# Performance work log

Hardware: AMD Instinct MI355X
Metric: run time of the kernel (lower is better)

## Reference

```python
import jax, jax.numpy as jnp
import numpy as np

B, T, V, H = 32, 256, 16, 256


def _layer_norm(x, g, b, eps=1e-5):
    m = jnp.mean(x, axis=-1, keepdims=True)
    v = jnp.mean(jnp.square(x - m), axis=-1, keepdims=True)
    return (x - m) * jax.lax.rsqrt(v + eps) * g + b


def setup_inputs() -> dict:
    keys = iter(jax.random.split(jax.random.key(0), 16))

    def nrm(shape, s=0.02):
        return (jax.random.normal(next(keys), shape, dtype=jnp.float32) * s).astype(jnp.float32)

    return {
        "x": nrm((B, T, V, H), 1.0),
        "context": nrm((B, T, H), 1.0),
        "joint_Wa": nrm((V * H, H)),
        "joint_ba": jnp.zeros((H,), jnp.float32),
        "joint_Wc": nrm((H, H)),
        "joint_Wi": nrm((H, H)),
        "joint_bi": jnp.zeros((H,), jnp.float32),
        "joint_Wglu": nrm((H, 2 * V)),
        "joint_bglu": jnp.zeros((2 * V,), jnp.float32),
        "joint_Wskip": nrm((V * H, V)),
        "joint_bskip": jnp.zeros((V,), jnp.float32),
        "joint_ln_g": jnp.ones((V,), jnp.float32),
        "joint_ln_b": jnp.zeros((V,), jnp.float32),
        "var_Wa": nrm((V, H, H)),
        "var_ba": jnp.zeros((V, H), jnp.float32),
        "var_Wi": nrm((V, H, H)),
        "var_bi": jnp.zeros((V, H), jnp.float32),
        "var_Wglu": nrm((V, H, 2 * H)),
        "var_bglu": jnp.zeros((V, 2 * H), jnp.float32),
        "var_ln_g": jnp.ones((V, H), jnp.float32),
        "var_ln_b": jnp.zeros((V, H), jnp.float32),
    }


def reference(x, context, joint_Wa, joint_ba, joint_Wc, joint_Wi, joint_bi,
              joint_Wglu, joint_bglu, joint_Wskip, joint_bskip,
              joint_ln_g, joint_ln_b,
              var_Wa, var_ba, var_Wi, var_bi, var_Wglu, var_bglu,
              var_ln_g, var_ln_b):
    b, t, v, h = x.shape
    Xi = x.reshape(b, t, v * h)  # flatten last two dims

    # ---- joint GRN (with context) producing variable logits [b,t,v] ----
    a = Xi @ joint_Wa + joint_ba + context @ joint_Wc
    a = jax.nn.elu(a)
    i = a @ joint_Wi + joint_bi
    g = i @ joint_Wglu + joint_bglu
    g1, g2 = jnp.split(g, 2, axis=-1)  # GLU: first half gated by sigmoid(second)
    glu_out = g1 * jax.nn.sigmoid(g2)
    skip = Xi @ joint_Wskip + joint_bskip  # out_size != in_size -> skip projection
    sparse_weights = jax.nn.softmax(_layer_norm(glu_out + skip, joint_ln_g, joint_ln_b), axis=-1)

    # ---- per-variable GRNs, batched over the variable axis ----
    av = jax.nn.elu(jnp.einsum('btvh,vhk->btvk', x, var_Wa) + var_ba)
    iv = jnp.einsum('btvh,vhk->btvk', av, var_Wi) + var_bi
    gv = jnp.einsum('btvh,vhd->btvd', iv, var_Wglu) + var_bglu
    gv1, gv2 = jnp.split(gv, 2, axis=-1)
    tv = _layer_norm(gv1 * jax.nn.sigmoid(gv2) + x, var_ln_g, var_ln_b)  # [b,t,v,h]

    # stack(dim=-1) + matmul with weights == weighted sum over variables
    variable_ctx = jnp.einsum('btvh,btv->bth', tv, sparse_weights)
    return variable_ctx, sparse_weights
```

## Files before the change

### kernel.cpp

```cpp
#include <hip/hip_runtime.h>

typedef unsigned short u16;
typedef __attribute__((ext_vector_type(8))) __bf16 bf16x8;
typedef __attribute__((ext_vector_type(4))) float f32x4;
typedef __attribute__((ext_vector_type(8))) u16 u16x8;

__device__ __forceinline__ u16 f2b(float f) {
  union { float f; unsigned u; } v; v.f = f;
  return (u16)((v.u + 0x7fffu + ((v.u >> 16) & 1u)) >> 16);
}
__device__ __forceinline__ float b2f(u16 h) {
  union { unsigned u; float f; } v; v.u = ((unsigned)h) << 16;
  return v.f;
}
__device__ __forceinline__ f32x4 mfma16(bf16x8 a, bf16x8 b, f32x4 c) {
  return __builtin_amdgcn_mfma_f32_16x16x32_bf16(a, b, c, 0, 0, 0);
}
__device__ __forceinline__ void gl_lds16(const void* g, void* l) {
  __builtin_amdgcn_global_load_lds(
      (const __attribute__((address_space(1))) void*)g,
      (__attribute__((address_space(3))) void*)l, 16, 0, 0);
}
__device__ __forceinline__ u16x8 cvt8(float4 a, float4 b) {
  u16x8 o;
  o[0] = f2b(a.x); o[1] = f2b(a.y); o[2] = f2b(a.z); o[3] = f2b(a.w);
  o[4] = f2b(b.x); o[5] = f2b(b.y); o[6] = f2b(b.z); o[7] = f2b(b.w);
  return o;
}
__device__ __forceinline__ u16x8 cvt8v(f32x4 a, f32x4 b) {
  u16x8 o;
  o[0] = f2b(a[0]); o[1] = f2b(a[1]); o[2] = f2b(a[2]); o[3] = f2b(a[3]);
  o[4] = f2b(b[0]); o[5] = f2b(b[1]); o[6] = f2b(b[2]); o[7] = f2b(b[3]);
  return o;
}

__global__ __launch_bounds__(256) void transpose_cast(
    const float* __restrict__ src, u16* __restrict__ dst,
    int R, int C, int dstStride, long srcBatch, long dstBatch)
{
  __shared__ float tile[32][33];
  src += (long)blockIdx.z * srcBatch;
  dst += (long)blockIdx.z * dstBatch;
  const int c0 = blockIdx.x * 32, r0 = blockIdx.y * 32;
  const int tx = threadIdx.x & 31, ty = threadIdx.x >> 5;
  for (int i = ty; i < 32; i += 8) {
    int r = r0 + i, cc = c0 + tx;
    if (r < R && cc < C) tile[i][tx] = src[(long)r * C + cc];
  }
  __syncthreads();
  for (int i = ty; i < 32; i += 8) {
    int cc = c0 + i, r = r0 + tx;
    if (cc < C && r < R) dst[(long)cc * dstStride + r] = f2b(tile[tx][i]);
  }
}

__global__ __launch_bounds__(256) void var_w_prep(
    const float* __restrict__ W, u16* __restrict__ dstbase, int rbase)
{
  const int v = blockIdx.x;
  const int kc = blockIdx.y;
  const int n = threadIdx.x;
  const float* src = W + (size_t)v * 65536 + (size_t)kc * 64 * 256 + n;
  u16* dst = dstbase + (size_t)v * 262144 + (size_t)(rbase + kc) * 16384;
#pragma unroll
  for (int l = 0; l < 8; ++l) {
    u16x8 o;
#pragma unroll
    for (int e = 0; e < 8; ++e) o[e] = f2b(src[(l * 8 + e) * 256]);
    const int chunk = n * 8 + (l ^ (n & 7));
    *(u16x8*)&dst[chunk * 8] = o;
  }
}

__global__ __launch_bounds__(256) void var_wglu_prep(
    const float* __restrict__ W, u16* __restrict__ dstbase)
{
  const int v = blockIdx.x;
  const int kc = blockIdx.y;
  u16* dst = dstbase + (size_t)v * 262144 + (size_t)(8 + kc) * 16384;
#pragma unroll
  for (int half = 0; half < 2; ++half) {
    const int n = threadIdx.x + half * 256;
    const float* src = W + (size_t)v * 131072 + (size_t)kc * 32 * 512 + n;
    const int s = n >> 1;
#pragma unroll
    for (int l = 0; l < 4; ++l) {
      u16x8 o;
#pragma unroll
      for (int e = 0; e < 8; ++e) o[e] = f2b(src[(l * 8 + e) * 512]);
      const int chunk = s * 8 + ((((n & 1) * 4 + l)) ^ (s & 7));
      *(u16x8*)&dst[chunk * 8] = o;
    }
  }
}

#define K1TOT 4352
__global__ __launch_bounds__(256, 3) void gemm1(
    const float* __restrict__ x, const float* __restrict__ ctx,
    const u16* __restrict__ bt1, const float* __restrict__ ba,
    const float* __restrict__ bskip, u16* __restrict__ a_bf, float* __restrict__ skip_f)
{
  __shared__ u16 As[32 * 64];
  __shared__ u16 Bs[288 * 64];
  const int tid = threadIdx.x;
  const int n0 = blockIdx.x * 32;
  const int w = tid >> 6, lane = tid & 63;
  const int q = lane >> 4, c = lane & 15;
  const int rt = w & 1, cg = w >> 1;
  const int t0 = cg ? 9 : 0;
  const int nt = cg ? 8 : 9;

  f32x4 acc[9];
#pragma unroll
  for (int i = 0; i < 9; ++i) acc[i] = f32x4{0.f, 0.f, 0.f, 0.f};

  const int sr = tid >> 3, sp = tid & 7;
  const int sl = sp ^ (sr & 7);

  for (int kb = 0; kb < K1TOT; kb += 64) {
    {
      const float* s = (kb < 4096)
          ? (x + (size_t)(n0 + sr) * 4096 + kb + sl * 8)
          : (ctx + (size_t)(n0 + sr) * 256 + (kb - 4096) + sl * 8);
      float4 v0 = ((const float4*)s)[0];
      float4 v1 = ((const float4*)s)[1];
      *(u16x8*)&As[tid * 8] = cvt8(v0, v1);
    }
#pragma unroll
    for (int i = 0; i < 9; ++i) {
      const int cb = (i * 4 + w) * 64;
      const int cid = cb + lane;
      const int row = cid >> 3, p = cid & 7;
      const int l = p ^ (row & 7);
      const u16* src = (row < 272) ? (bt1 + (size_t)row * K1TOT + kb + l * 8) : bt1;
      gl_lds16(src, &Bs[cb * 8]);
    }
    __syncthreads();
#pragma unroll
    for (int kk = 0; kk < 2; ++kk) {
      const int arow = rt * 16 + c;
      bf16x8 af = *(const bf16x8*)&As[(arow * 64 + kk * 32 + q * 8) ^ ((arow & 7) << 3)];
#pragma unroll
      for (int ti = 0; ti < 9; ++ti) {
        if (ti < nt) {
          const int n16 = (t0 + ti) * 16 + c;
          bf16x8 bfr = *(const bf16x8*)&Bs[(n16 * 64 + kk * 32 + q * 8) ^ ((n16 & 7) << 3)];
          acc[ti] = mfma16(af, bfr, acc[ti]);
        }
      }
    }
    __syncthreads();
  }
#pragma unroll
  for (int ti = 0; ti < 9; ++ti) {
    if (ti < nt) {
      const int col = (t0 + ti) * 16 + c;
#pragma unroll
      for (int j = 0; j < 4; ++j) {
        const long n = n0 + rt * 16 + q * 4 + j;
        float vv = acc[ti][j];
        if (col < 256) {
          vv += ba[col];
          vv = vv > 0.f ? vv : expm1f(vv);
          a_bf[n * 256 + col] = f2b(vv);
        } else {
          skip_f[n * 16 + (col - 256)] = vv + bskip[col - 256];
        }
      }
    }
  }
}

__global__ __launch_bounds__(256, 3) void gemm_i(
    const u16* __restrict__ a_bf, const u16* __restrict__ wiT,
    const float* __restrict__ bi, u16* __restrict__ i_bf)
{
  __shared__ u16 As[32 * 64];
  __shared__ u16 Bs[256 * 64];
  const int tid = threadIdx.x;
  const int n0 = blockIdx.x * 32;
  const int w = tid >> 6, lane = tid & 63;
  const int q = lane >> 4, c = lane & 15;
  const int rt = w & 1, cg = w >> 1;

  f32x4 acc[8];
#pragma unroll
  for (int i = 0; i < 8; ++i) acc[i] = f32x4{0.f, 0.f, 0.f, 0.f};

  for (int kb = 0; kb < 256; kb += 64) {
    {
      const int row = tid >> 3, p = tid & 7;
      const int l = p ^ (row & 7);
      gl_lds16(a_bf + (size_t)(n0 + row) * 256 + kb + l * 8, &As[w * 512]);
    }
#pragma unroll
    for (int i = 0; i < 8; ++i) {
      const int cb = (i * 4 + w) * 64;
      const int cid = cb + lane;
      const int row = cid >> 3, p = cid & 7;
      const int l = p ^ (row & 7);
      gl_lds16(wiT + (size_t)row * 256 + kb + l * 8, &Bs[cb * 8]);
    }
    __syncthreads();
#pragma unroll
    for (int kk = 0; kk < 2; ++kk) {
      const int arow = rt * 16 + c;
      bf16x8 af = *(const bf16x8*)&As[(arow * 64 + kk * 32 + q * 8) ^ ((arow & 7) << 3)];
#pragma unroll
      for (int ti = 0; ti < 8; ++ti) {
        const int n16 = (cg * 8 + ti) * 16 + c;
        bf16x8 bfr = *(const bf16x8*)&Bs[(n16 * 64 + kk * 32 + q * 8) ^ ((n16 & 7) << 3)];
        acc[ti] = mfma16(af, bfr, acc[ti]);
      }
    }
    __syncthreads();
  }
#pragma unroll
  for (int ti = 0; ti < 8; ++ti) {
    const int col = (cg * 8 + ti) * 16 + c;
    const float bb = bi[col];
#pragma unroll
    for (int j = 0; j < 4; ++j) {
      const long n = n0 + rt * 16 + q * 4 + j;
      i_bf[n * 256 + col] = f2b(acc[ti][j] + bb);
    }
  }
}

__global__ __launch_bounds__(256) void joint_tail(
    const u16* __restrict__ i_bf, const u16* __restrict__ wgluT,
    const float* __restrict__ bglu, const float* __restrict__ skip_f,
    const float* __restrict__ lng, const float* __restrict__ lnb,
    float* __restrict__ swout)
{
  __shared__ float wlds[32 * 257];
  __shared__ float ilds[4][256];
  const int tid = threadIdx.x;
  for (int jj = 0; jj < 32; ++jj) wlds[jj * 257 + tid] = b2f(wgluT[jj * 256 + tid]);
  const int w = tid >> 6, lane = tid & 63;
  const long n = (long)blockIdx.x * 4 + w;
  {
    const u16* src = i_bf + n * 256 + lane * 4;
    float4 f;
    f.x = b2f(src[0]); f.y = b2f(src[1]); f.z = b2f(src[2]); f.w = b2f(src[3]);
    *(float4*)&ilds[w][lane * 4] = f;
  }
  __syncthreads();
  const int cc32 = lane & 31;
  const int k0 = (lane >> 5) * 128;
  float acc = 0.f;
  for (int k = 0; k < 128; ++k) acc += ilds[w][k0 + k] * wlds[cc32 * 257 + k0 + k];
  acc += __shfl_xor(acc, 32, 64);
  const float gfull = acc + bglu[cc32];
  const int cc = lane & 15;
  const float g1 = __shfl(gfull, cc, 64);
  const float g2 = __shfl(gfull, cc + 16, 64);
  const float glu = g1 / (1.f + __expf(-g2));
  const float y = glu + skip_f[n * 16 + cc];
  float s = y, ss = y * y;
#pragma unroll
  for (int d = 1; d < 16; d <<= 1) { s += __shfl_xor(s, d, 64); ss += __shfl_xor(ss, d, 64); }
  const float m = s * (1.f / 16.f);
  const float var = ss * (1.f / 16.f) - m * m;
  const float t = (y - m) * rsqrtf(var + 1e-5f) * lng[cc] + lnb[cc];
  float mx = t;
#pragma unroll
  for (int d = 1; d < 16; d <<= 1) mx = fmaxf(mx, __shfl_xor(mx, d, 64));
  const float e = __expf(t - mx);
  float es = e;
#pragma unroll
  for (int d = 1; d < 16; d <<= 1) es += __shfl_xor(es, d, 64);
  if (lane < 16) swout[n * 16 + lane] = e / es;
}

__global__ __launch_bounds__(256) void reduce4(
    const float* __restrict__ part, float* __restrict__ out)
{
  const size_t i = ((size_t)blockIdx.x * 256 + threadIdx.x) * 4;
  float4 a = *(const float4*)(part + i);
  float4 b = *(const float4*)(part + i + 2097152);
  float4 c = *(const float4*)(part + i + 4194304);
  float4 d = *(const float4*)(part + i + 6291456);
  float4 o;
  o.x = a.x + b.x + c.x + d.x;
  o.y = a.y + b.y + c.y + d.y;
  o.z = a.z + b.z + c.z + d.z;
  o.w = a.w + b.w + c.w + d.w;
  *(float4*)(out + i) = o;
}

__global__ __launch_bounds__(1024, 1) void var_chain(
    const float* __restrict__ x, const u16* __restrict__ varw,
    const float* __restrict__ vba, const float* __restrict__ vbi,
    const float* __restrict__ vbglu, const float* __restrict__ vlng,
    const float* __restrict__ vlnb, const float* __restrict__ sw,
    float* __restrict__ outp)
{
  extern __shared__ u16 smem[];
  u16* const xt1 = smem;
  u16* const wtb = smem + 32768;
  float* const red   = (float*)(smem + 65536);
  float* const muinv = red + 1024;

  const int tid = threadIdx.x;
  const int w = tid >> 6, lane = tid & 63;
  const int q = lane >> 4, c = lane & 15;
  const int rt = w >> 2, cg = w & 3;
  const int vbase = blockIdx.x * 4;
  const int n0 = blockIdx.y * 128;

  f32x4 outacc[2][4];
#pragma unroll
  for (int p = 0; p < 2; ++p)
#pragma unroll
    for (int u = 0; u < 4; ++u) outacc[p][u] = f32x4{0.f, 0.f, 0.f, 0.f};

  auto STAGE = [&](int b, int tn) {
    const u16* tb = varw + (size_t)(vbase + (tn >> 4)) * 262144 + (size_t)(tn & 15) * 16384;
    u16* dst = wtb + (b << 14);
#pragma unroll
    for (int i = 0; i < 2; ++i) {
      const int cb = (i * 16 + w) * 64;
      gl_lds16(tb + (size_t)(cb + lane) * 8, dst + (size_t)cb * 8);
    }
  };
  auto XSTAGE = [&](int v) {
#pragma unroll
    for (int jj = 0; jj < 4; ++jj) {
      const int cid = jj * 1024 + tid;
      const int r = cid >> 5, p = cid & 31;
      const int l = (p & 24) | ((p & 7) ^ (r & 7));
      const f32x4* s = (const f32x4*)(x + (size_t)(n0 + r) * 4096 + (size_t)v * 256 + l * 8);
      f32x4 v0 = __builtin_nontemporal_load(s);
      f32x4 v1 = __builtin_nontemporal_load(s + 1);
      *(u16x8*)&xt1[cid * 8] = cvt8v(v0, v1);
    }
  };

  auto ROUND_TAIL = [&](int t) {
    __builtin_amdgcn_s_barrier();
    __builtin_amdgcn_sched_barrier(0);
    STAGE(t & 1, (t + 2 < 64) ? t + 2 : 63);
    __builtin_amdgcn_sched_barrier(0);
    asm volatile("s_waitcnt vmcnt(2)" ::: "memory");
    __builtin_amdgcn_sched_barrier(0);
    __builtin_amdgcn_s_barrier();
    __builtin_amdgcn_sched_barrier(0);
  };

  STAGE(0, 0);
  STAGE(1, 1);
  XSTAGE(vbase);
  __syncthreads();

  int t = 0;
  for (int vi = 0; vi < 4; ++vi) {
    const int v = vbase + vi;

    f32x4 acc2[2][4];
#pragma unroll
    for (int p = 0; p < 2; ++p)
#pragma unroll
      for (int ti = 0; ti < 4; ++ti) acc2[p][ti] = f32x4{0.f, 0.f, 0.f, 0.f};

    for (int kc = 0; kc < 4; ++kc, ++t) {
      const u16* wcur = wtb + ((t & 1) << 14);
      __builtin_amdgcn_s_setprio(1);
#pragma unroll
      for (int kk = 0; kk < 2; ++kk) {
        bf16x8 a[2];
#pragma unroll
        for (int p = 0; p < 2; ++p) {
          const int r = (rt * 2 + p) * 16 + c;
          a[p] = *(const bf16x8*)&xt1[(r * 256 + kc * 64 + kk * 32 + q * 8) ^ ((r & 7) << 3)];
        }
#pragma unroll
        for (int ti = 0; ti < 4; ++ti) {
          const int n16 = (cg * 4 + ti) * 16 + c;
          bf16x8 b = *(const bf16x8*)&wcur[(n16 * 64 + kk * 32 + q * 8) ^ ((n16 & 7) << 3)];
          acc2[0][ti] = mfma16(a[0], b, acc2[0][ti]);
          acc2[1][ti] = mfma16(a[1], b, acc2[1][ti]);
        }
      }
      __builtin_amdgcn_s_setprio(0);
      ROUND_TAIL(t);
    }
#pragma unroll
    for (int p = 0; p < 2; ++p)
#pragma unroll
      for (int ti = 0; ti < 4; ++ti) {
        const int col = (cg * 4 + ti) * 16 + c;
        const float bb = vba[v * 256 + col];
#pragma unroll
        for (int j = 0; j < 4; ++j) {
          const int row = (rt * 2 + p) * 16 + q * 4 + j;
          float vv = acc2[p][ti][j] + bb;
          vv = vv > 0.f ? vv : expm1f(vv);
          xt1[(row * 256 + col) ^ ((row & 7) << 3)] = f2b(vv);
        }
      }
    __syncthreads();

#pragma unroll
    for (int p = 0; p < 2; ++p)
#pragma unroll
      for (int ti = 0; ti < 4; ++ti) acc2[p][ti] = f32x4{0.f, 0.f, 0.f, 0.f};
    for (int kc = 0; kc < 4; ++kc, ++t) {
      const u16* wcur = wtb + ((t & 1) << 14);
      __builtin_amdgcn_s_setprio(1);
#pragma unroll
      for (int kk = 0; kk < 2; ++kk) {
        bf16x8 a[2];
#pragma unroll
        for (int p = 0; p < 2; ++p) {
          const int r = (rt * 2 + p) * 16 + c;
          a[p] = *(const bf16x8*)&xt1[(r * 256 + kc * 64 + kk * 32 + q * 8) ^ ((r & 7) << 3)];
        }
#pragma unroll
        for (int ti = 0; ti < 4; ++ti) {
          const int n16 = (cg * 4 + ti) * 16 + c;
          bf16x8 b = *(const bf16x8*)&wcur[(n16 * 64 + kk * 32 + q * 8) ^ ((n16 & 7) << 3)];
          acc2[0][ti] = mfma16(a[0], b, acc2[0][ti]);
          acc2[1][ti] = mfma16(a[1], b, acc2[1][ti]);
        }
      }
      __builtin_amdgcn_s_setprio(0);
      ROUND_TAIL(t);
    }
#pragma unroll
    for (int p = 0; p < 2; ++p)
#pragma unroll
      for (int ti = 0; ti < 4; ++ti) {
        const int col = (cg * 4 + ti) * 16 + c;
        const float bb = vbi[v * 256 + col];
#pragma unroll
        for (int j = 0; j < 4; ++j) {
          const int row = (rt * 2 + p) * 16 + q * 4 + j;
          xt1[(row * 256 + col) ^ ((row & 7) << 3)] = f2b(acc2[p][ti][j] + bb);
        }
      }
    __syncthreads();

    f32x4 acc3[2][8];
#pragma unroll
    for (int p = 0; p < 2; ++p)
#pragma unroll
      for (int u = 0; u < 8; ++u) acc3[p][u] = f32x4{0.f, 0.f, 0.f, 0.f};
    for (int kc = 0; kc < 8; ++kc, ++t) {
      const u16* wcur = wtb + ((t & 1) << 14);
      bf16x8 a[2];
#pragma unroll
      for (int p = 0; p < 2; ++p) {
        const int r = (rt * 2 + p) * 16 + c;
        a[p] = *(const bf16x8*)&xt1[(r * 256 + kc * 32 + q * 8) ^ ((r & 7) << 3)];
      }
      __builtin_amdgcn_s_setprio(1);
#pragma unroll
      for (int u = 0; u < 8; ++u) {
        const int ct = cg * 4 + (u & 3) + ((u >> 2) << 4);
        const int n = ct * 16 + c;
        const int idx = (n >> 1) * 64 + ((((n & 1) * 4 + q) ^ ((n >> 1) & 7)) * 8);
        bf16x8 b = *(const bf16x8*)&wcur[idx];
        acc3[0][u] = mfma16(a[0], b, acc3[0][u]);
        acc3[1][u] = mfma16(a[1], b, acc3[1][u]);
      }
      __builtin_amdgcn_s_setprio(0);
      ROUND_TAIL(t);
    }

    float b1v[4], b2v[4], lgv[4], lbv[4];
#pragma unroll
    for (int u = 0; u < 4; ++u) {
      const int col = cg * 64 + u * 16 + c;
      b1v[u] = vbglu[v * 512 + col];
      b2v[u] = vbglu[v * 512 + 256 + col];
      lgv[u] = vlng[v * 256 + col];
      lbv[u] = vlnb[v * 256 + col];
    }
    float rs[2][4], rss[2][4];
#pragma unroll
    for (int p = 0; p < 2; ++p)
#pragma unroll
      for (int j = 0; j < 4; ++j) { rs[p][j] = 0.f; rss[p][j] = 0.f; }
#pragma unroll
    for (int p = 0; p < 2; ++p)
#pragma unroll
      for (int u = 0; u < 4; ++u) {
        const int col = cg * 64 + u * 16 + c;
#pragma unroll
        for (int j = 0; j < 4; ++j) {
          const int row = (rt * 2 + p) * 16 + q * 4 + j;
          const float g1 = acc3[p][u][j] + b1v[u];
          const float g2 = acc3[p][u + 4][j] + b2v[u];
          const float glu = g1 / (1.f + __expf(-g2));
          const float resid = __builtin_nontemporal_load(
              &x[(size_t)(n0 + row) * 4096 + (size_t)v * 256 + col]);
          const float r = glu + resid;
          acc3[p][u][j] = r;
          rs[p][j] += r; rss[p][j] += r * r;
        }
      }
#pragma unroll
    for (int p = 0; p < 2; ++p)
#pragma unroll
      for (int j = 0; j < 4; ++j)
#pragma unroll
        for (int d = 1; d < 16; d <<= 1) {
          rs[p][j]  += __shfl_xor(rs[p][j], d, 64);
          rss[p][j] += __shfl_xor(rss[p][j], d, 64);
        }
    if (c == 0) {
#pragma unroll
      for (int p = 0; p < 2; ++p)
#pragma unroll
        for (int j = 0; j < 4; ++j) {
          const int row = (rt * 2 + p) * 16 + q * 4 + j;
          red[row * 8 + cg * 2]     = rs[p][j];
          red[row * 8 + cg * 2 + 1] = rss[p][j];
        }
    }
    __syncthreads();
    if (tid < 128) {
      float ms = 0.f, vs = 0.f;
#pragma unroll
      for (int ww = 0; ww < 4; ++ww) { ms += red[tid * 8 + ww * 2]; vs += red[tid * 8 + ww * 2 + 1]; }
      const float mm = ms * (1.f / 256.f);
      muinv[tid * 2]     = mm;
      muinv[tid * 2 + 1] = rsqrtf(vs * (1.f / 256.f) - mm * mm + 1e-5f);
    }
    __syncthreads();
#pragma unroll
    for (int p = 0; p < 2; ++p) {
#pragma unroll
      for (int j = 0; j < 4; ++j) {
        const int row = (rt * 2 + p) * 16 + q * 4 + j;
        const float mu = muinv[row * 2], inv = muinv[row * 2 + 1];
        const float wv = sw[(size_t)(n0 + row) * 16 + v];
#pragma unroll
        for (int u = 0; u < 4; ++u) {
          const float tv = (acc3[p][u][j] - mu) * inv * lgv[u] + lbv[u];
          outacc[p][u][j] += tv * wv;
        }
      }
    }
    __syncthreads();
    if (vi < 3) {
      XSTAGE(v + 1);
      __syncthreads();
    }
  }

  float* const dst = outp + (size_t)blockIdx.x * 2097152;
#pragma unroll
  for (int p = 0; p < 2; ++p)
#pragma unroll
    for (int u = 0; u < 4; ++u) {
      const int col = cg * 64 + u * 16 + c;
#pragma unroll
      for (int j = 0; j < 4; ++j) {
        const int row = (rt * 2 + p) * 16 + q * 4 + j;
        dst[(size_t)(n0 + row) * 256 + col] = outacc[p][u][j];
      }
    }
}

extern "C" void kernel_launch(void* const* d_in, const int* in_sizes, int n_in,
                              void* d_out, int out_size, void* d_ws, size_t ws_size,
                              hipStream_t stream) {
  const float* x     = (const float*)d_in[0];
  const float* ctx   = (const float*)d_in[1];
  const float* jWa   = (const float*)d_in[2];
  const float* jba   = (const float*)d_in[3];
  const float* jWc   = (const float*)d_in[4];
  const float* jWi   = (const float*)d_in[5];
  const float* jbi   = (const float*)d_in[6];
  const float* jWglu = (const float*)d_in[7];
  const float* jbglu = (const float*)d_in[8];
  const float* jWskip= (const float*)d_in[9];
  const float* jbskip= (const float*)d_in[10];
  const float* jlng  = (const float*)d_in[11];
  const float* jlnb  = (const float*)d_in[12];
  const float* vWa   = (const float*)d_in[13];
  const float* vba   = (const float*)d_in[14];
  const float* vWi   = (const float*)d_in[15];
  const float* vbi   = (const float*)d_in[16];
  const float* vWglu = (const float*)d_in[17];
  const float* vbglu = (const float*)d_in[18];
  const float* vlng  = (const float*)d_in[19];
  const float* vlnb  = (const float*)d_in[20];
  float* out = (float*)d_out;

  char* ws = (char*)d_ws;
  size_t off = 0;
  auto alloc = [&](size_t bytes) { void* p = ws + off; off += (bytes + 255) & ~(size_t)255; return p; };
  u16* bt1     = (u16*)alloc((size_t)272 * 4352 * 2);
  u16* wiT     = (u16*)alloc((size_t)256 * 256 * 2);
  u16* wgluT   = (u16*)alloc((size_t)32 * 256 * 2);
  u16* varw    = (u16*)alloc((size_t)16 * 262144 * 2);
  u16* a_bf    = (u16*)alloc((size_t)8192 * 256 * 2);
  u16* i_bf    = (u16*)alloc((size_t)8192 * 256 * 2);
  float* skipf = (float*)alloc((size_t)8192 * 16 * 4);
  float* outp  = (float*)alloc((size_t)4 * 8192 * 256 * 4);

  hipMemsetAsync(bt1, 0, (size_t)272 * 4352 * 2, stream);

  dim3 blk(256);
  transpose_cast<<<dim3(8, 128, 1),  blk, 0, stream>>>(jWa,   bt1,              4096, 256, 4352, 0, 0);
  transpose_cast<<<dim3(8, 8, 1),    blk, 0, stream>>>(jWc,   bt1 + 4096,       256,  256, 4352, 0, 0);
  transpose_cast<<<dim3(1, 128, 1),  blk, 0, stream>>>(jWskip,bt1 + 256 * 4352, 4096, 16,  4352, 0, 0);
  transpose_cast<<<dim3(8, 8, 1),    blk, 0, stream>>>(jWi,   wiT,   256, 256, 256, 0, 0);
  transpose_cast<<<dim3(1, 8, 1),    blk, 0, stream>>>(jWglu, wgluT, 256, 32,  256, 0, 0);
  var_w_prep<<<dim3(16, 4), blk, 0, stream>>>(vWa, varw, 0);
  var_w_prep<<<dim3(16, 4), blk, 0, stream>>>(vWi, varw, 4);
  var_wglu_prep<<<dim3(16, 8), blk, 0, stream>>>(vWglu, varw);

  gemm1<<<dim3(256), blk, 0, stream>>>(x, ctx, bt1, jba, jbskip, a_bf, skipf);
  gemm_i<<<dim3(256), blk, 0, stream>>>(a_bf, wiT, jbi, i_bf);
  joint_tail<<<dim3(2048), blk, 0, stream>>>(i_bf, wgluT, jbglu, skipf, jlng, jlnb,
                                             out + (size_t)8192 * 256);

  hipFuncSetAttribute((const void*)var_chain, hipFuncAttributeMaxDynamicSharedMemorySize, 136192);
  var_chain<<<dim3(4, 64), dim3(1024), 136192, stream>>>(x, varw, vba, vbi, vbglu,
                                                         vlng, vlnb,
                                                         out + (size_t)8192 * 256, outp);
  reduce4<<<dim3(2048), blk, 0, stream>>>(outp, out);
}
```

Measured before the change: 470.1 us.

## Halve var_chain row tile, use 32-wide K weight tiles with triple buffering

Restructures the per-variable GRN kernel to process 64 rows per block instead of 128, doubling the grid to 512 blocks. Weight tiles are re-laid out by a unified prep kernel into 32-deep K chunks, staged through a three-slot LDS ring instead of two. Warps are rearranged to 2 row groups by 8 column groups. The aim is lower LDS use (86KB) and more blocks in flight to hide latency. The cost is more weight reloads from L2 per row and more barrier rounds per block.

Result: slower. 661.5 us (+40.7%).

```diff
diff --git a/kernel.cpp b/kernel.cpp
--- a/kernel.cpp
+++ b/kernel.cpp
@@ -54,43 +54,23 @@
   }
 }
 
-__global__ __launch_bounds__(256) void var_w_prep(
-    const float* __restrict__ W, u16* __restrict__ dstbase, int rbase)
+__global__ __launch_bounds__(256) void var_prep_half(
+    const float* __restrict__ W, u16* __restrict__ dstbase,
+    int srcN, int colOff, int tileBase, int tileStep)
 {
   const int v = blockIdx.x;
   const int kc = blockIdx.y;
   const int n = threadIdx.x;
-  const float* src = W + (size_t)v * 65536 + (size_t)kc * 64 * 256 + n;
-  u16* dst = dstbase + (size_t)v * 262144 + (size_t)(rbase + kc) * 16384;
-#pragma unroll
-  for (int l = 0; l < 8; ++l) {
+  const float* src = W + (size_t)v * 256 * srcN + (size_t)(kc * 32) * srcN + colOff + n;
+  u16* dst = dstbase + (size_t)v * 262144 + (size_t)(tileBase + kc * tileStep) * 8192;
+  const int sw = (n >> 1) & 3;
+#pragma unroll
+  for (int l = 0; l < 4; ++l) {
     u16x8 o;
 #pragma unroll
-    for (int e = 0; e < 8; ++e) o[e] = f2b(src[(l * 8 + e) * 256]);
-    const int chunk = n * 8 + (l ^ (n & 7));
+    for (int e = 0; e < 8; ++e) o[e] = f2b(src[(l * 8 + e) * srcN]);
+    const int chunk = n * 4 + (l ^ sw);
     *(u16x8*)&dst[chunk * 8] = o;
-  }
-}
-
-__global__ __launch_bounds__(256) void var_wglu_prep(
-    const float* __restrict__ W, u16* __restrict__ dstbase)
-{
-  const int v = blockIdx.x;
-  const int kc = blockIdx.y;
-  u16* dst = dstbase + (size_t)v * 262144 + (size_t)(8 + kc) * 16384;
-#pragma unroll
-  for (int half = 0; half < 2; ++half) {
-    const int n = threadIdx.x + half * 256;
-    const float* src = W + (size_t)v * 131072 + (size_t)kc * 32 * 512 + n;
-    const int s = n >> 1;
-#pragma unroll
-    for (int l = 0; l < 4; ++l) {
-      u16x8 o;
-#pragma unroll
-      for (int e = 0; e < 8; ++e) o[e] = f2b(src[(l * 8 + e) * 512]);
-      const int chunk = s * 8 + ((((n & 1) * 4 + l)) ^ (s & 7));
-      *(u16x8*)&dst[chunk * 8] = o;
-    }
   }
 }
 
@@ -298,35 +278,31 @@
 {
   extern __shared__ u16 smem[];
   u16* const xt1 = smem;
-  u16* const wtb = smem + 32768;
-  float* const red   = (float*)(smem + 65536);
+  u16* const wtb = smem + 16384;
+  float* const red   = (float*)(smem + 40960);
   float* const muinv = red + 1024;
 
   const int tid = threadIdx.x;
   const int w = tid >> 6, lane = tid & 63;
   const int q = lane >> 4, c = lane & 15;
-  const int rt = w >> 2, cg = w & 3;
+  const int rt = w >> 3, cg = w & 7;
   const int vbase = blockIdx.x * 4;
-  const int n0 = blockIdx.y * 128;
-
-  f32x4 outacc[2][4];
+  const int n0 = blockIdx.y * 64;
+  const int bsw = q ^ ((c >> 1) & 3);
+
+  f32x4 outacc[2][2];
 #pragma unroll
   for (int p = 0; p < 2; ++p)
 #pragma unroll
-    for (int u = 0; u < 4; ++u) outacc[p][u] = f32x4{0.f, 0.f, 0.f, 0.f};
+    for (int u = 0; u < 2; ++u) outacc[p][u] = f32x4{0.f, 0.f, 0.f, 0.f};
 
   auto STAGE = [&](int b, int tn) {
-    const u16* tb = varw + (size_t)(vbase + (tn >> 4)) * 262144 + (size_t)(tn & 15) * 16384;
-    u16* dst = wtb + (b << 14);
-#pragma unroll
-    for (int i = 0; i < 2; ++i) {
-      const int cb = (i * 16 + w) * 64;
-      gl_lds16(tb + (size_t)(cb + lane) * 8, dst + (size_t)cb * 8);
-    }
+    const u16* tb = varw + (size_t)(vbase + (tn >> 5)) * 262144 + (size_t)(tn & 31) * 8192;
+    gl_lds16(tb + (size_t)(w * 64 + lane) * 8, wtb + b * 8192 + w * 512);
   };
   auto XSTAGE = [&](int v) {
 #pragma unroll
-    for (int jj = 0; jj < 4; ++jj) {
+    for (int jj = 0; jj < 2; ++jj) {
       const int cid = jj * 1024 + tid;
       const int r = cid >> 5, p = cid & 31;
       const int l = (p & 24) | ((p & 7) ^ (r & 7));
@@ -336,20 +312,24 @@
       *(u16x8*)&xt1[cid * 8] = cvt8v(v0, v1);
     }
   };
-
   auto ROUND_TAIL = [&](int t) {
     __builtin_amdgcn_s_barrier();
     __builtin_amdgcn_sched_barrier(0);
-    STAGE(t & 1, (t + 2 < 64) ? t + 2 : 63);
+    STAGE(t % 3, (t + 3 < 128) ? t + 3 : 127);
     __builtin_amdgcn_sched_barrier(0);
     asm volatile("s_waitcnt vmcnt(2)" ::: "memory");
     __builtin_amdgcn_sched_barrier(0);
     __builtin_amdgcn_s_barrier();
     __builtin_amdgcn_sched_barrier(0);
   };
+  auto BREAD = [&](const u16* wcur, int ct) -> bf16x8 {
+    const int nn = ct * 16 + c;
+    return *(const bf16x8*)&wcur[nn * 32 + bsw * 8];
+  };
 
   STAGE(0, 0);
   STAGE(1, 1);
+  STAGE(2, 2);
   XSTAGE(vbase);
   __syncthreads();
 
@@ -357,30 +337,27 @@
   for (int vi = 0; vi < 4; ++vi) {
     const int v = vbase + vi;
 
-    f32x4 acc2[2][4];
-#pragma unroll
-    for (int p = 0; p < 2; ++p)
-#pragma unroll
-      for (int ti = 0; ti < 4; ++ti) acc2[p][ti] = f32x4{0.f, 0.f, 0.f, 0.f};
-
-    for (int kc = 0; kc < 4; ++kc, ++t) {
-      const u16* wcur = wtb + ((t & 1) << 14);
+    f32x4 acc2[2][2];
+#pragma unroll
+    for (int p = 0; p < 2; ++p)
+#pragma unroll
+      for (int u = 0; u < 2; ++u) acc2[p][u] = f32x4{0.f, 0.f, 0.f, 0.f};
+
+    for (int r = 0; r < 8; ++r, ++t) {
+      const u16* wcur = wtb + (t % 3) * 8192;
+      const int k0 = r * 32 + q * 8;
       __builtin_amdgcn_s_setprio(1);
-#pragma unroll
-      for (int kk = 0; kk < 2; ++kk) {
-        bf16x8 a[2];
-#pragma unroll
-        for (int p = 0; p < 2; ++p) {
-          const int r = (rt * 2 + p) * 16 + c;
-          a[p] = *(const bf16x8*)&xt1[(r * 256 + kc * 64 + kk * 32 + q * 8) ^ ((r & 7) << 3)];
-        }
-#pragma unroll
-        for (int ti = 0; ti < 4; ++ti) {
-          const int n16 = (cg * 4 + ti) * 16 + c;
-          bf16x8 b = *(const bf16x8*)&wcur[(n16 * 64 + kk * 32 + q * 8) ^ ((n16 & 7) << 3)];
-          acc2[0][ti] = mfma16(a[0], b, acc2[0][ti]);
-          acc2[1][ti] = mfma16(a[1], b, acc2[1][ti]);
-        }
+      bf16x8 a[2];
+#pragma unroll
+      for (int p = 0; p < 2; ++p) {
+        const int row = rt * 32 + p * 16 + c;
+        a[p] = *(const bf16x8*)&xt1[(row * 256 + k0) ^ ((row & 7) << 3)];
+      }
+#pragma unroll
+      for (int u = 0; u < 2; ++u) {
+        bf16x8 b = BREAD(wcur, cg * 2 + u);
+        acc2[0][u] = mfma16(a[0], b, acc2[0][u]);
+        acc2[1][u] = mfma16(a[1], b, acc2[1][u]);
       }
       __builtin_amdgcn_s_setprio(0);
       ROUND_TAIL(t);
@@ -388,13 +365,13 @@
 #pragma unroll
     for (int p = 0; p < 2; ++p)
 #pragma unroll
-      for (int ti = 0; ti < 4; ++ti) {
-        const int col = (cg * 4 + ti) * 16 + c;
+      for (int u = 0; u < 2; ++u) {
+        const int col = (cg * 2 + u) * 16 + c;
         const float bb = vba[v * 256 + col];
 #pragma unroll
         for (int j = 0; j < 4; ++j) {
-          const int row = (rt * 2 + p) * 16 + q * 4 + j;
-          float vv = acc2[p][ti][j] + bb;
+          const int row = rt * 32 + p * 16 + q * 4 + j;
+          float vv = acc2[p][u][j] + bb;
           vv = vv > 0.f ? vv : expm1f(vv);
           xt1[(row * 256 + col) ^ ((row & 7) << 3)] = f2b(vv);
         }
@@ -404,25 +381,22 @@
 #pragma unroll
     for (int p = 0; p < 2; ++p)
 #pragma unroll
-      for (int ti = 0; ti < 4; ++ti) acc2[p][ti] = f32x4{0.f, 0.f, 0.f, 0.f};
-    for (int kc = 0; kc < 4; ++kc, ++t) {
-      const u16* wcur = wtb + ((t & 1) << 14);
+      for (int u = 0; u < 2; ++u) acc2[p][u] = f32x4{0.f, 0.f, 0.f, 0.f};
+    for (int r = 0; r < 8; ++r, ++t) {
+      const u16* wcur = wtb + (t % 3) * 8192;
+      const int k0 = r * 32 + q * 8;
       __builtin_amdgcn_s_setprio(1);
-#pragma unroll
-      for (int kk = 0; kk < 2; ++kk) {
-        bf16x8 a[2];
-#pragma unroll
-        for (int p = 0; p < 2; ++p) {
-          const int r = (rt * 2 + p) * 16 + c;
-          a[p] = *(const bf16x8*)&xt1[(r * 256 + kc * 64 + kk * 32 + q * 8) ^ ((r & 7) << 3)];
-        }
-#pragma unroll
-        for (int ti = 0; ti < 4; ++ti) {
-          const int n16 = (cg * 4 + ti) * 16 + c;
-          bf16x8 b = *(const bf16x8*)&wcur[(n16 * 64 + kk * 32 + q * 8) ^ ((n16 & 7) << 3)];
-          acc2[0][ti] = mfma16(a[0], b, acc2[0][ti]);
-          acc2[1][ti] = mfma16(a[1], b, acc2[1][ti]);
-        }
+      bf16x8 a[2];
+#pragma unroll
+      for (int p = 0; p < 2; ++p) {
+        const int row = rt * 32 + p * 16 + c;
+        a[p] = *(const bf16x8*)&xt1[(row * 256 + k0) ^ ((row & 7) << 3)];
+      }
+#pragma unroll
+      for (int u = 0; u < 2; ++u) {
+        bf16x8 b = BREAD(wcur, cg * 2 + u);
+        acc2[0][u] = mfma16(a[0], b, acc2[0][u]);
+        acc2[1][u] = mfma16(a[1], b, acc2[1][u]);
       }
       __builtin_amdgcn_s_setprio(0);
       ROUND_TAIL(t);
@@ -430,48 +404,47 @@
 #pragma unroll
     for (int p = 0; p < 2; ++p)
 #pragma unroll
-      for (int ti = 0; ti < 4; ++ti) {
-        const int col = (cg * 4 + ti) * 16 + c;
+      for (int u = 0; u < 2; ++u) {
+        const int col = (cg * 2 + u) * 16 + c;
         const float bb = vbi[v * 256 + col];
 #pragma unroll
         for (int j = 0; j < 4; ++j) {
-          const int row = (rt * 2 + p) * 16 + q * 4 + j;
-          xt1[(row * 256 + col) ^ ((row & 7) << 3)] = f2b(acc2[p][ti][j] + bb);
-        }
-      }
-    __syncthreads();
-
-    f32x4 acc3[2][8];
-#pragma unroll
-    for (int p = 0; p < 2; ++p)
-#pragma unroll
-      for (int u = 0; u < 8; ++u) acc3[p][u] = f32x4{0.f, 0.f, 0.f, 0.f};
-    for (int kc = 0; kc < 8; ++kc, ++t) {
-      const u16* wcur = wtb + ((t & 1) << 14);
+          const int row = rt * 32 + p * 16 + q * 4 + j;
+          xt1[(row * 256 + col) ^ ((row & 7) << 3)] = f2b(acc2[p][u][j] + bb);
+        }
+      }
+    __syncthreads();
+
+    f32x4 acc3[2][4];
+#pragma unroll
+    for (int p = 0; p < 2; ++p)
+#pragma unroll
+      for (int u = 0; u < 4; ++u) acc3[p][u] = f32x4{0.f, 0.f, 0.f, 0.f};
+    for (int r = 0; r < 16; ++r, ++t) {
+      const u16* wcur = wtb + (t % 3) * 8192;
+      const int kc = r >> 1, half = r & 1;
+      const int k0 = kc * 32 + q * 8;
+      __builtin_amdgcn_s_setprio(1);
       bf16x8 a[2];
 #pragma unroll
       for (int p = 0; p < 2; ++p) {
-        const int r = (rt * 2 + p) * 16 + c;
-        a[p] = *(const bf16x8*)&xt1[(r * 256 + kc * 32 + q * 8) ^ ((r & 7) << 3)];
-      }
-      __builtin_amdgcn_s_setprio(1);
-#pragma unroll
-      for (int u = 0; u < 8; ++u) {
-        const int ct = cg * 4 + (u & 3) + ((u >> 2) << 4);
-        const int n = ct * 16 + c;
-        const int idx = (n >> 1) * 64 + ((((n & 1) * 4 + q) ^ ((n >> 1) & 7)) * 8);
-        bf16x8 b = *(const bf16x8*)&wcur[idx];
-        acc3[0][u] = mfma16(a[0], b, acc3[0][u]);
-        acc3[1][u] = mfma16(a[1], b, acc3[1][u]);
+        const int row = rt * 32 + p * 16 + c;
+        a[p] = *(const bf16x8*)&xt1[(row * 256 + k0) ^ ((row & 7) << 3)];
+      }
+#pragma unroll
+      for (int u = 0; u < 2; ++u) {
+        bf16x8 b = BREAD(wcur, cg * 2 + u);
+        acc3[0][(half << 1) | u] = mfma16(a[0], b, acc3[0][(half << 1) | u]);
+        acc3[1][(half << 1) | u] = mfma16(a[1], b, acc3[1][(half << 1) | u]);
       }
       __builtin_amdgcn_s_setprio(0);
       ROUND_TAIL(t);
     }
 
-    float b1v[4], b2v[4], lgv[4], lbv[4];
-#pragma unroll
-    for (int u = 0; u < 4; ++u) {
-      const int col = cg * 64 + u * 16 + c;
+    float b1v[2], b2v[2], lgv[2], lbv[2];
+#pragma unroll
+    for (int u = 0; u < 2; ++u) {
+      const int col = (cg * 2 + u) * 16 + c;
       b1v[u] = vbglu[v * 512 + col];
       b2v[u] = vbglu[v * 512 + 256 + col];
       lgv[u] = vlng[v * 256 + col];
@@ -485,19 +458,19 @@
 #pragma unroll
     for (int p = 0; p < 2; ++p)
 #pragma unroll
-      for (int u = 0; u < 4; ++u) {
-        const int col = cg * 64 + u * 16 + c;
+      for (int u = 0; u < 2; ++u) {
+        const int col = (cg * 2 + u) * 16 + c;
 #pragma unroll
         for (int j = 0; j < 4; ++j) {
-          const int row = (rt * 2 + p) * 16 + q * 4 + j;
+          const int row = rt * 32 + p * 16 + q * 4 + j;
           const float g1 = acc3[p][u][j] + b1v[u];
-          const float g2 = acc3[p][u + 4][j] + b2v[u];
+          const float g2 = acc3[p][2 + u][j] + b2v[u];
           const float glu = g1 / (1.f + __expf(-g2));
           const float resid = __builtin_nontemporal_load(
               &x[(size_t)(n0 + row) * 4096 + (size_t)v * 256 + col]);
-          const float r = glu + resid;
-          acc3[p][u][j] = r;
-          rs[p][j] += r; rss[p][j] += r * r;
+          const float rr = glu + resid;
+          acc3[p][u][j] = rr;
+          rs[p][j] += rr; rss[p][j] += rr * rr;
         }
       }
 #pragma unroll
@@ -514,16 +487,16 @@
       for (int p = 0; p < 2; ++p)
 #pragma unroll
         for (int j = 0; j < 4; ++j) {
-          const int row = (rt * 2 + p) * 16 + q * 4 + j;
-          red[row * 8 + cg * 2]     = rs[p][j];
-          red[row * 8 + cg * 2 + 1] = rss[p][j];
-        }
-    }
-    __syncthreads();
-    if (tid < 128) {
+          const int row = rt * 32 + p * 16 + q * 4 + j;
+          red[row * 16 + cg * 2]     = rs[p][j];
+          red[row * 16 + cg * 2 + 1] = rss[p][j];
+        }
+    }
+    __syncthreads();
+    if (tid < 64) {
       float ms = 0.f, vs = 0.f;
 #pragma unroll
-      for (int ww = 0; ww < 4; ++ww) { ms += red[tid * 8 + ww * 2]; vs += red[tid * 8 + ww * 2 + 1]; }
+      for (int ww = 0; ww < 8; ++ww) { ms += red[tid * 16 + ww * 2]; vs += red[tid * 16 + ww * 2 + 1]; }
       const float mm = ms * (1.f / 256.f);
       muinv[tid * 2]     = mm;
       muinv[tid * 2 + 1] = rsqrtf(vs * (1.f / 256.f) - mm * mm + 1e-5f);
@@ -533,11 +506,11 @@
     for (int p = 0; p < 2; ++p) {
 #pragma unroll
       for (int j = 0; j < 4; ++j) {
-        const int row = (rt * 2 + p) * 16 + q * 4 + j;
+        const int row = rt * 32 + p * 16 + q * 4 + j;
         const float mu = muinv[row * 2], inv = muinv[row * 2 + 1];
         const float wv = sw[(size_t)(n0 + row) * 16 + v];
 #pragma unroll
-        for (int u = 0; u < 4; ++u) {
+        for (int u = 0; u < 2; ++u) {
           const float tv = (acc3[p][u][j] - mu) * inv * lgv[u] + lbv[u];
           outacc[p][u][j] += tv * wv;
         }
@@ -554,11 +527,11 @@
 #pragma unroll
   for (int p = 0; p < 2; ++p)
 #pragma unroll
-    for (int u = 0; u < 4; ++u) {
-      const int col = cg * 64 + u * 16 + c;
+    for (int u = 0; u < 2; ++u) {
+      const int col = (cg * 2 + u) * 16 + c;
 #pragma unroll
       for (int j = 0; j < 4; ++j) {
-        const int row = (rt * 2 + p) * 16 + q * 4 + j;
+        const int row = rt * 32 + p * 16 + q * 4 + j;
         dst[(size_t)(n0 + row) * 256 + col] = outacc[p][u][j];
       }
     }
@@ -610,17 +583,18 @@
   transpose_cast<<<dim3(1, 128, 1),  blk, 0, stream>>>(jWskip,bt1 + 256 * 4352, 4096, 16,  4352, 0, 0);
   transpose_cast<<<dim3(8, 8, 1),    blk, 0, stream>>>(jWi,   wiT,   256, 256, 256, 0, 0);
   transpose_cast<<<dim3(1, 8, 1),    blk, 0, stream>>>(jWglu, wgluT, 256, 32,  256, 0, 0);
-  var_w_prep<<<dim3(16, 4), blk, 0, stream>>>(vWa, varw, 0);
-  var_w_prep<<<dim3(16, 4), blk, 0, stream>>>(vWi, varw, 4);
-  var_wglu_prep<<<dim3(16, 8), blk, 0, stream>>>(vWglu, varw);
+  var_prep_half<<<dim3(16, 8), blk, 0, stream>>>(vWa,   varw, 256, 0,   0,  1);
+  var_prep_half<<<dim3(16, 8), blk, 0, stream>>>(vWi,   varw, 256, 0,   8,  1);
+  var_prep_half<<<dim3(16, 8), blk, 0, stream>>>(vWglu, varw, 512, 0,   16, 2);
+  var_prep_half<<<dim3(16, 8), blk, 0, stream>>>(vWglu, varw, 512, 256, 17, 2);
 
   gemm1<<<dim3(256), blk, 0, stream>>>(x, ctx, bt1, jba, jbskip, a_bf, skipf);
   gemm_i<<<dim3(256), blk, 0, stream>>>(a_bf, wiT, jbi, i_bf);
   joint_tail<<<dim3(2048), blk, 0, stream>>>(i_bf, wgluT, jbglu, skipf, jlng, jlnb,
                                              out + (size_t)8192 * 256);
 
-  hipFuncSetAttribute((const void*)var_chain, hipFuncAttributeMaxDynamicSharedMemorySize, 136192);
-  var_chain<<<dim3(4, 64), dim3(1024), 136192, stream>>>(x, varw, vba, vbi, vbglu,
+  hipFuncSetAttribute((const void*)var_chain, hipFuncAttributeMaxDynamicSharedMemorySize, 86528);
+  var_chain<<<dim3(4, 128), dim3(1024), 86528, stream>>>(x, varw, vba, vbi, vbglu,
                                                          vlng, vlnb,
                                                          out + (size_t)8192 * 256, outp);
   reduce4<<<dim3(2048), blk, 0, stream>>>(outp, out);
```
